# Kernel tuning notes

Hardware: AMD Instinct MI355X
Metric: run time of the kernel (lower is better)

The kernel has to match this reference:

```python
import jax, jax.numpy as jnp
import numpy as np

N = 50000
E = 800000
IN = 256
OUT = 32
H1 = 8
NEG_SLOPE = 0.2


def setup_inputs() -> dict:
    key = jax.random.key(0)
    ks = jax.random.split(key, 12)
    x = jax.random.normal(ks[0], (N, IN), dtype=jnp.float32)
    src = jax.random.randint(ks[1], (E,), 0, N, dtype=jnp.int32)
    dst = jax.random.randint(ks[2], (E,), 0, N, dtype=jnp.int32)
    s1 = 1.0 / np.sqrt(IN)
    s2 = 1.0 / np.sqrt(H1 * OUT)
    # layer 1 (8 heads, residual = Identity since IN == H1*OUT)
    W1 = jax.random.normal(ks[3], (IN, H1 * OUT), dtype=jnp.float32) * s1
    al1 = jax.random.normal(ks[4], (H1, OUT), dtype=jnp.float32) * s1
    ar1 = jax.random.normal(ks[5], (H1, OUT), dtype=jnp.float32) * s1
    b1 = jnp.zeros((H1 * OUT,), dtype=jnp.float32)
    # layer 2 (1 head, residual = Linear since H1*OUT != OUT)
    W2 = jax.random.normal(ks[6], (H1 * OUT, OUT), dtype=jnp.float32) * s2
    al2 = jax.random.normal(ks[7], (1, OUT), dtype=jnp.float32) * s2
    ar2 = jax.random.normal(ks[8], (1, OUT), dtype=jnp.float32) * s2
    resW2 = jax.random.normal(ks[9], (H1 * OUT, OUT), dtype=jnp.float32) * s2
    b2 = jnp.zeros((OUT,), dtype=jnp.float32)
    return {"x": x, "src": src, "dst": dst, "W1": W1, "al1": al1, "ar1": ar1,
            "b1": b1, "W2": W2, "al2": al2, "ar2": ar2, "resW2": resW2, "b2": b2}


def gat_layer(x, src, dst, W, al, ar, bias, heads, out_feats, res_fn):
    # x: (N, in). feat: (N, H, D)
    feat = (x @ W).reshape(N, heads, out_feats)
    el = jnp.sum(feat * al[None], axis=-1)  # (N, H)
    er = jnp.sum(feat * ar[None], axis=-1)  # (N, H)
    e = jax.nn.leaky_relu(el[src] + er[dst], NEG_SLOPE)  # (E, H)
    # edge softmax over incoming edges of each destination node
    emax = jax.ops.segment_max(e, dst, num_segments=N)  # (N, H)
    ee = jnp.exp(e - emax[dst])
    esum = jax.ops.segment_sum(ee, dst, num_segments=N)  # (N, H)
    a = ee / esum[dst]  # (E, H)
    # gather-multiply-scatter-add aggregation
    msg = feat[src] * a[..., None]  # (E, H, D)
    rst = jax.ops.segment_sum(msg, dst, num_segments=N)  # (N, H, D)
    rst = rst + res_fn(x)
    rst = rst + bias.reshape(1, heads, out_feats)
    return rst


def reference(x, src, dst, W1, al1, ar1, b1, W2, al2, ar2, resW2, b2):
    # layer 1: 8 heads, residual Identity (IN == H1*OUT)
    y = gat_layer(x, src, dst, W1, al1, ar1, b1, H1, OUT,
                  lambda h: h.reshape(N, H1, OUT))
    y = jax.nn.relu(y).reshape(N, H1 * OUT)
    # layer 2: 1 head, residual Linear projection
    y = gat_layer(y, src, dst, W2, al2, ar2, b2, 1, OUT,
                  lambda h: (h @ resW2).reshape(N, 1, OUT))
    return y
```

## Files before the change

### kernel.cpp

```cpp
#include <hip/hip_runtime.h>
#include <hip/hip_bf16.h>
#include <hip/hip_fp8.h>

#define N_NODES 50000
#define M_PAD   50048
#define N_EDGES 800000
#define NEG_SLOPE 0.2f

#define EPT 8
#define BKA 391
#define NBUCK 256
#define NPB 196
#define SEGCAP 40
#define GBLK 782

typedef __attribute__((ext_vector_type(8))) short bf16x8;
typedef __attribute__((ext_vector_type(4))) float f32x4;
typedef __attribute__((ext_vector_type(2))) float f32x2;

__device__ __forceinline__ unsigned short f2bf(float f) {
    unsigned u = __float_as_uint(f);
    u += 0x7FFFu + ((u >> 16) & 1u);
    return (unsigned short)(u >> 16);
}
__device__ __forceinline__ float bf2f(unsigned short h) {
    return __uint_as_float(((unsigned)h) << 16);
}

#if __has_builtin(__builtin_amdgcn_cvt_pk_f32_fp8)
__device__ __forceinline__ f32x2 fp8pk_lo(unsigned int p) { return __builtin_amdgcn_cvt_pk_f32_fp8(p, false); }
__device__ __forceinline__ f32x2 fp8pk_hi(unsigned int p) { return __builtin_amdgcn_cvt_pk_f32_fp8(p, true); }
#else
__device__ __forceinline__ float fp82f_s(unsigned char b) {
    __hip_fp8_e4m3 t; t.__x = (__hip_fp8_storage_t)b; return (float)t;
}
__device__ __forceinline__ f32x2 fp8pk_lo(unsigned int p) {
    f32x2 r; r.x = fp82f_s(p & 0xff); r.y = fp82f_s((p >> 8) & 0xff); return r;
}
__device__ __forceinline__ f32x2 fp8pk_hi(unsigned int p) {
    f32x2 r; r.x = fp82f_s((p >> 16) & 0xff); r.y = fp82f_s(p >> 24); return r;
}
#endif

#if __has_builtin(__builtin_amdgcn_cvt_pk_fp8_f32)
__device__ __forceinline__ unsigned int fp8enc2(float a, float b) {
    return (unsigned int)__builtin_amdgcn_cvt_pk_fp8_f32(a, b, 0, false);
}
#else
__device__ __forceinline__ unsigned int fp8enc2(float a, float b) {
    __hip_fp8_e4m3 ta(a), tb(b);
    return (unsigned int)ta.__x | ((unsigned int)tb.__x << 8);
}
#endif


__global__ __launch_bounds__(256) void k_trans(const float* __restrict__ W1, const float* __restrict__ W2,
                                               const float* __restrict__ resW2, const float* __restrict__ x,
                                               unsigned short* __restrict__ W1T, unsigned short* __restrict__ W2T,
                                               unsigned short* __restrict__ xb, unsigned int* __restrict__ btot) {
    int flat = blockIdx.y * 10 + blockIdx.x;
    if (flat == 0) btot[threadIdx.x] = 0;

    if (blockIdx.y < 8) {
        __shared__ unsigned short tile[32][33];
        int bx = blockIdx.x;
        const float* in;
        unsigned short* out;
        int Nn, n0;
        if (bx < 8)      { in = W1;    out = W1T;            Nn = 256; n0 = bx * 32; }
        else if (bx == 8){ in = W2;    out = W2T;            Nn = 32;  n0 = 0; }
        else             { in = resW2; out = W2T + 32 * 256; Nn = 32;  n0 = 0; }
        int k0 = blockIdx.y * 32;
        int tx = threadIdx.x & 31, ty = threadIdx.x >> 5;
        #pragma unroll
        for (int r = 0; r < 4; ++r) {
            int k = k0 + ty + r * 8;
            tile[ty + r * 8][tx] = f2bf(in[(size_t)k * Nn + n0 + tx]);
        }
        __syncthreads();
        #pragma unroll
        for (int r = 0; r < 4; ++r) {
            int n = ty + r * 8;
            out[(size_t)(n0 + n) * 256 + k0 + tx] = tile[tx][n];
        }
    } else {
        int xid = flat - 80;
        const size_t NCHUNK = (size_t)M_PAD * 256 / 8;
        for (size_t c = (size_t)xid * 256 + threadIdx.x; c < NCHUNK; c += (size_t)720 * 256) {
            size_t base = c * 8;
            float4 a = make_float4(0.f, 0.f, 0.f, 0.f), b = a;
            if (base < (size_t)N_NODES * 256) {
                a = *(const float4*)(x + base);
                b = *(const float4*)(x + base + 4);
            }
            ushort4 h0, h1;
            h0.x = f2bf(a.x); h0.y = f2bf(a.y); h0.z = f2bf(a.z); h0.w = f2bf(a.w);
            h1.x = f2bf(b.x); h1.y = f2bf(b.y); h1.z = f2bf(b.z); h1.w = f2bf(b.w);
            *(ushort4*)(xb + base) = h0;
            *(ushort4*)(xb + base + 4) = h1;
        }
    }
}


__device__ __forceinline__ void gemm1_half(int g, int bn0,
                                           const unsigned short* __restrict__ xb,
                                           const unsigned short* __restrict__ BT,
                                           const float* __restrict__ al1, const float* __restrict__ ar1,
                                           unsigned char* __restrict__ Cb8,
                                           float* __restrict__ el1, float* __restrict__ er1) {
    const int t = threadIdx.x;
    const int bm0 = g * 64;
    const int wave = t >> 6, lane = t & 63;
    const int wm = (wave & 1) * 32, wn = (wave >> 1) * 64;
    const int lm = lane & 15, quad = lane >> 4;

    f32x4 acc[2][4];
    #pragma unroll
    for (int i = 0; i < 2; ++i)
        #pragma unroll
        for (int j = 0; j < 4; ++j)
            #pragma unroll
            for (int r = 0; r < 4; ++r) acc[i][j][r] = 0.f;

    const unsigned short* bp[4];
    const unsigned short* ap[2];
    #pragma unroll
    for (int i = 0; i < 4; ++i)
        bp[i] = BT + (size_t)(bn0 + wn + i * 16 + lm) * 256 + quad * 8;
    #pragma unroll
    for (int i = 0; i < 2; ++i)
        ap[i] = xb + (size_t)(bm0 + wm + i * 16 + lm) * 256 + quad * 8;

    bf16x8 nb[4], na[2];
    #pragma unroll
    for (int i = 0; i < 4; ++i) nb[i] = *(const bf16x8*)(bp[i]);
    #pragma unroll
    for (int i = 0; i < 2; ++i) na[i] = *(const bf16x8*)(ap[i]);

    #pragma unroll
    for (int k0 = 0; k0 < 256; k0 += 32) {
        bf16x8 cb[4], ca[2];
        #pragma unroll
        for (int i = 0; i < 4; ++i) cb[i] = nb[i];
        #pragma unroll
        for (int i = 0; i < 2; ++i) ca[i] = na[i];
        if (k0 + 32 < 256) {
            #pragma unroll
            for (int i = 0; i < 4; ++i) nb[i] = *(const bf16x8*)(bp[i] + k0 + 32);
            #pragma unroll
            for (int i = 0; i < 2; ++i) na[i] = *(const bf16x8*)(ap[i] + k0 + 32);
        }
        #pragma unroll
        for (int mi = 0; mi < 2; ++mi)
            #pragma unroll
            for (int ni = 0; ni < 4; ++ni)
                acc[mi][ni] = __builtin_amdgcn_mfma_f32_16x16x32_bf16(ca[mi], cb[ni], acc[mi][ni], 0, 0, 0);
    }

    #pragma unroll
    for (int mi = 0; mi < 2; ++mi) {
        #pragma unroll
        for (int ni = 0; ni < 4; ++ni) {
            int col = bn0 + wn + ni * 16 + lm;
            int row0 = bm0 + wm + mi * 16 + quad * 4;
            unsigned int p01 = fp8enc2(acc[mi][ni][0], acc[mi][ni][1]);
            unsigned int p23 = fp8enc2(acc[mi][ni][2], acc[mi][ni][3]);
            Cb8[(size_t)(row0 + 0) * 256 + col] = (unsigned char)(p01 & 0xff);
            Cb8[(size_t)(row0 + 1) * 256 + col] = (unsigned char)((p01 >> 8) & 0xff);
            Cb8[(size_t)(row0 + 2) * 256 + col] = (unsigned char)(p23 & 0xff);
            Cb8[(size_t)(row0 + 3) * 256 + col] = (unsigned char)((p23 >> 8) & 0xff);
        }
    }
    float alv[4], arv[4];
    #pragma unroll
    for (int ni = 0; ni < 4; ++ni) {
        int colg = bn0 + wn + ni * 16 + lm;
        alv[ni] = al1[colg];
        arv[ni] = ar1[colg];
    }
    int head0 = (bn0 + wn) >> 5;
    #pragma unroll
    for (int gg = 0; gg < 2; ++gg) {
        #pragma unroll
        for (int mi = 0; mi < 2; ++mi) {
            #pragma unroll
            for (int r = 0; r < 4; ++r) {
                float pel = acc[mi][2 * gg][r] * alv[2 * gg] + acc[mi][2 * gg + 1][r] * alv[2 * gg + 1];
                float per = acc[mi][2 * gg][r] * arv[2 * gg] + acc[mi][2 * gg + 1][r] * arv[2 * gg + 1];
                #pragma unroll
                for (int m = 1; m <= 8; m <<= 1) {
                    pel += __shfl_xor(pel, m, 64);
                    per += __shfl_xor(per, m, 64);
                }
                if (lm == 0) {
                    int row = bm0 + wm + mi * 16 + quad * 4 + r;
                    el1[row * 8 + head0 + gg] = pel;
                    er1[row * 8 + head0 + gg] = per;
                }
            }
        }
    }
}


__global__ __launch_bounds__(512) void k_gemm1(const unsigned short* __restrict__ xb,
                                               const unsigned short* __restrict__ BT,
                                               const float* __restrict__ al1, const float* __restrict__ ar1,
                                               unsigned char* __restrict__ Cb8,
                                               float* __restrict__ el1, float* __restrict__ er1) {
    gemm1_half(blockIdx.x, 0, xb, BT, al1, ar1, Cb8, el1, er1);
}


__global__ __launch_bounds__(256) void k_bucketA(const int* __restrict__ src, const int* __restrict__ dst,
                                                 uint2* __restrict__ seg, unsigned int* __restrict__ cnt,
                                                 unsigned int* __restrict__ btot) {
    __shared__ unsigned int lcnt[NBUCK];
    int vb = blockIdx.x;
    lcnt[threadIdx.x] = 0;
    __syncthreads();
    int base = vb * (256 * EPT) + threadIdx.x;
    int sv[EPT], dv[EPT], bk[EPT], lr[EPT];
    #pragma unroll
    for (int q = 0; q < EPT; ++q) {
        int i = base + q * 256;
        if (i < N_EDGES) { sv[q] = src[i]; dv[q] = dst[i]; }
        else dv[q] = -1;
    }
    #pragma unroll
    for (int q = 0; q < EPT; ++q) {
        if (dv[q] >= 0) {
            bk[q] = (int)((unsigned)dv[q] / NPB);
            lr[q] = atomicAdd(&lcnt[bk[q]], 1u);
        }
    }
    __syncthreads();
    cnt[vb * NBUCK + threadIdx.x] = lcnt[threadIdx.x];
    if (lcnt[threadIdx.x] > 0) atomicAdd(&btot[threadIdx.x], lcnt[threadIdx.x]);
    #pragma unroll
    for (int q = 0; q < EPT; ++q) {
        if (dv[q] >= 0 && lr[q] < SEGCAP) {
            size_t slot = ((size_t)bk[q] * BKA + vb) * SEGCAP + lr[q];
            seg[slot] = make_uint2((unsigned)sv[q], (unsigned)dv[q] - (unsigned)bk[q] * NPB);
        }
    }
}


__global__ __launch_bounds__(256) void k_bucketB(const uint2* __restrict__ seg, const unsigned int* __restrict__ cnt,
                                                 const unsigned int* __restrict__ btot,
                                                 int* __restrict__ rowoff, int* __restrict__ csr_src) {
    __shared__ unsigned int hist[NPB];
    __shared__ unsigned int cursor[NPB];
    __shared__ unsigned int red[256];
    int b = blockIdx.x;
    int t = threadIdx.x;
    if (t < NPB) hist[t] = 0;
    red[t] = (t < b) ? btot[t] : 0;
    __syncthreads();
    #pragma unroll
    for (int off = 128; off > 0; off >>= 1) {
        if (t < off) red[t] += red[t + off];
        __syncthreads();
    }
    unsigned int base = red[0];
    __syncthreads();
    for (int s = t; s < BKA; s += 256) {
        unsigned int c = cnt[s * NBUCK + b];
        const uint2* sp = seg + ((size_t)b * BKA + s) * SEGCAP;
        for (unsigned int j = 0; j < c; ++j) {
            atomicAdd(&hist[sp[j].y], 1u);
        }
    }
    __syncthreads();
    red[t] = (t < NPB) ? hist[t] : 0;
    __syncthreads();
    for (int off = 1; off < 256; off <<= 1) {
        unsigned int val = (t >= off) ? red[t - off] : 0;
        __syncthreads();
        red[t] += val;
        __syncthreads();
    }
    if (t < NPB) {
        unsigned int excl = red[t] - hist[t];
        cursor[t] = excl;
        int v = b * NPB + t;
        if (v < N_NODES) rowoff[v] = (int)(base + excl);
    }
    if (b == NBUCK - 1 && t == 0) rowoff[N_NODES] = N_EDGES;
    __syncthreads();
    for (int s = t; s < BKA; s += 256) {
        unsigned int c = cnt[s * NBUCK + b];
        const uint2* sp = seg + ((size_t)b * BKA + s) * SEGCAP;
        for (unsigned int j = 0; j < c; ++j) {
            uint2 eg = sp[j];
            unsigned int r = atomicAdd(&cursor[eg.y], 1u);
            csr_src[base + r] = (int)eg.x;
        }
    }
}


__global__ __launch_bounds__(256) void k_agg1(const unsigned char* __restrict__ feat8,
                                              const float* __restrict__ el1, const float* __restrict__ er1,
                                              const unsigned short* __restrict__ xb, const float* __restrict__ b1,
                                              const int* __restrict__ rowoff, const int* __restrict__ csr_src,
                                              unsigned short* __restrict__ y_b) {
    int v = (blockIdx.x * 256 + threadIdx.x) >> 6;
    int lane = threadIdx.x & 63;
    if (v >= M_PAD) return;
    int c0 = lane * 4;
    if (v >= N_NODES) {
        ushort4 z = {0, 0, 0, 0};
        *(ushort4*)(y_b + (size_t)v * 256 + c0) = z;
        return;
    }
    int h = lane >> 3;
    float er  = er1[v * 8 + h];
    float erc = er1[v * 8 + (lane & 7)];
    float ax = 0.f, ay = 0.f, az = 0.f, aw = 0.f, wsum = 0.f;
    int s = rowoff[v], e = rowoff[v + 1];
    int j = s;
    for (; j + 7 < e; j += 8) {
        int um = csr_src[j + (lane >> 3)];
        float elv = el1[um * 8 + (lane & 7)];
        int u[8];
        #pragma unroll
        for (int q = 0; q < 8; ++q) u[q] = __shfl(um, q * 8);
        unsigned int hv[8];
        #pragma unroll
        for (int q = 0; q < 8; ++q) hv[q] = *(const unsigned int*)(feat8 + (size_t)u[q] * 256 + c0);
        float tq = elv + erc;
        tq = fmaxf(tq, NEG_SLOPE * tq);
        float wv = __expf(tq);
        #pragma unroll
        for (int q = 0; q < 8; ++q) {
            float w = __shfl(wv, q * 8 + h);
            wsum += w;
            f32x2 lo = fp8pk_lo(hv[q]);
            f32x2 hi = fp8pk_hi(hv[q]);
            ax += w * lo.x; ay += w * lo.y; az += w * hi.x; aw += w * hi.y;
        }
    }
    for (; j + 3 < e; j += 4) {
        int u[4];
        #pragma unroll
        for (int q = 0; q < 4; ++q) u[q] = csr_src[j + q];
        float tt[4];
        #pragma unroll
        for (int q = 0; q < 4; ++q) tt[q] = el1[u[q] * 8 + h] + er;
        unsigned int hv[4];
        #pragma unroll
        for (int q = 0; q < 4; ++q) hv[q] = *(const unsigned int*)(feat8 + (size_t)u[q] * 256 + c0);
        #pragma unroll
        for (int q = 0; q < 4; ++q) {
            float tq = fmaxf(tt[q], NEG_SLOPE * tt[q]);
            float w = __expf(tq);
            wsum += w;
            f32x2 lo = fp8pk_lo(hv[q]);
            f32x2 hi = fp8pk_hi(hv[q]);
            ax += w * lo.x; ay += w * lo.y; az += w * hi.x; aw += w * hi.y;
        }
    }
    for (; j < e; ++j) {
        int u = csr_src[j];
        float tt = el1[u * 8 + h] + er;
        unsigned int hh = *(const unsigned int*)(feat8 + (size_t)u * 256 + c0);
        tt = fmaxf(tt, NEG_SLOPE * tt);
        float w = __expf(tt);
        wsum += w;
        f32x2 lo = fp8pk_lo(hh);
        f32x2 hi = fp8pk_hi(hh);
        ax += w * lo.x; ay += w * lo.y; az += w * hi.x; aw += w * hi.y;
    }
    float inv = (e > s) ? 1.f / wsum : 0.f;
    ushort4 rh = *(const ushort4*)(xb + (size_t)v * 256 + c0);
    float4 bb = *(const float4*)(b1 + c0);
    ushort4 o;
    o.x = f2bf(fmaxf(ax * inv + bf2f(rh.x) + bb.x, 0.f));
    o.y = f2bf(fmaxf(ay * inv + bf2f(rh.y) + bb.y, 0.f));
    o.z = f2bf(fmaxf(az * inv + bf2f(rh.z) + bb.z, 0.f));
    o.w = f2bf(fmaxf(aw * inv + bf2f(rh.w) + bb.w, 0.f));
    *(ushort4*)(y_b + (size_t)v * 256 + c0) = o;
}


__global__ __launch_bounds__(256) void k_gemm2f(const unsigned short* __restrict__ Ab,
                                                const unsigned short* __restrict__ BT,
                                                const float* __restrict__ al2, const float* __restrict__ ar2,
                                                unsigned short* __restrict__ feat2b, float* __restrict__ res2,
                                                float* __restrict__ el2, float* __restrict__ er2) {
    const int t = threadIdx.x;
    const int bm0 = blockIdx.x * 64;
    const int wave = t >> 6, lane = t & 63;
    const int wm = (wave & 1) * 32, wn = (wave >> 1) * 32;
    const int lm = lane & 15, quad = lane >> 4;

    f32x4 acc[2][2];
    #pragma unroll
    for (int i = 0; i < 2; ++i)
        #pragma unroll
        for (int j = 0; j < 2; ++j)
            #pragma unroll
            for (int r = 0; r < 4; ++r) acc[i][j][r] = 0.f;

    const unsigned short* bp[2];
    const unsigned short* ap[2];
    #pragma unroll
    for (int i = 0; i < 2; ++i) {
        bp[i] = BT + (size_t)(wn + i * 16 + lm) * 256 + quad * 8;
        ap[i] = Ab + (size_t)(bm0 + wm + i * 16 + lm) * 256 + quad * 8;
    }

    bf16x8 nb[2], na[2];
    #pragma unroll
    for (int i = 0; i < 2; ++i) { nb[i] = *(const bf16x8*)(bp[i]); na[i] = *(const bf16x8*)(ap[i]); }

    #pragma unroll
    for (int k0 = 0; k0 < 256; k0 += 32) {
        bf16x8 cb[2], ca[2];
        #pragma unroll
        for (int i = 0; i < 2; ++i) { cb[i] = nb[i]; ca[i] = na[i]; }
        if (k0 + 32 < 256) {
            #pragma unroll
            for (int i = 0; i < 2; ++i) {
                nb[i] = *(const bf16x8*)(bp[i] + k0 + 32);
                na[i] = *(const bf16x8*)(ap[i] + k0 + 32);
            }
        }
        #pragma unroll
        for (int mi = 0; mi < 2; ++mi)
            #pragma unroll
            for (int ni = 0; ni < 2; ++ni)
                acc[mi][ni] = __builtin_amdgcn_mfma_f32_16x16x32_bf16(ca[mi], cb[ni], acc[mi][ni], 0, 0, 0);
    }

    #pragma unroll
    for (int mi = 0; mi < 2; ++mi) {
        #pragma unroll
        for (int ni = 0; ni < 2; ++ni) {
            int col = wn + ni * 16 + lm;
            #pragma unroll
            for (int r = 0; r < 4; ++r) {
                int row = bm0 + wm + mi * 16 + quad * 4 + r;
                float val = acc[mi][ni][r];
                if (col < 32) feat2b[(size_t)row * 32 + col] = f2bf(val);
                else          res2[(size_t)row * 32 + col - 32] = val;
            }
        }
    }
    if (wn == 0) {
        float alv[2], arv[2];
        #pragma unroll
        for (int ni = 0; ni < 2; ++ni) {
            alv[ni] = al2[ni * 16 + lm];
            arv[ni] = ar2[ni * 16 + lm];
        }
        #pragma unroll
        for (int mi = 0; mi < 2; ++mi) {
            #pragma unroll
            for (int r = 0; r < 4; ++r) {
                float pel = acc[mi][0][r] * alv[0] + acc[mi][1][r] * alv[1];
                float per = acc[mi][0][r] * arv[0] + acc[mi][1][r] * arv[1];
                #pragma unroll
                for (int m = 1; m <= 8; m <<= 1) {
                    pel += __shfl_xor(pel, m, 64);
                    per += __shfl_xor(per, m, 64);
                }
                if (lm == 0) {
                    int row = bm0 + wm + mi * 16 + quad * 4 + r;
                    el2[row] = pel;
                    er2[row] = per;
                }
            }
        }
    }
}


__global__ __launch_bounds__(256) void k_agg2(const unsigned short* __restrict__ feat2b,
                                              const float* __restrict__ el2, const float* __restrict__ er2,
                                              const float* __restrict__ res2, const float* __restrict__ b2,
                                              const int* __restrict__ rowoff, const int* __restrict__ csr_src,
                                              float* __restrict__ out) {
    int g = blockIdx.x * 256 + threadIdx.x;
    int v = g >> 5;
    int c = g & 31;
    if (v >= N_NODES) return;
    float er = er2[v];
    float acc = 0.f, wsum = 0.f;
    int s = rowoff[v], e = rowoff[v + 1];
    int j = s;
    for (; j + 3 < e; j += 4) {
        int u[4];
        #pragma unroll
        for (int q = 0; q < 4; ++q) u[q] = csr_src[j + q];
        float tt[4];
        #pragma unroll
        for (int q = 0; q < 4; ++q) tt[q] = el2[u[q]] + er;
        unsigned short fv[4];
        #pragma unroll
        for (int q = 0; q < 4; ++q) fv[q] = feat2b[(size_t)u[q] * 32 + c];
        #pragma unroll
        for (int q = 0; q < 4; ++q) {
            float tq = fmaxf(tt[q], NEG_SLOPE * tt[q]);
            float w = __expf(tq);
            wsum += w;
            acc += w * bf2f(fv[q]);
        }
    }
    for (; j < e; ++j) {
        int u = csr_src[j];
        float t = el2[u] + er;
        t = fmaxf(t, NEG_SLOPE * t);
        float w = __expf(t);
        wsum += w;
        acc += w * bf2f(feat2b[(size_t)u * 32 + c]);
    }
    float inv = (e > s) ? 1.f / wsum : 0.f;
    out[(size_t)v * 32 + c] = acc * inv + res2[(size_t)v * 32 + c] + b2[c];
}


extern "C" void kernel_launch(void* const* d_in, const int* in_sizes, int n_in,
                              void* d_out, int out_size, void* d_ws, size_t ws_size,
                              hipStream_t stream) {
    const float* x     = (const float*)d_in[0];
    const int*   src   = (const int*)d_in[1];
    const int*   dst   = (const int*)d_in[2];
    const float* W1    = (const float*)d_in[3];
    const float* al1   = (const float*)d_in[4];
    const float* ar1   = (const float*)d_in[5];
    const float* b1    = (const float*)d_in[6];
    const float* W2    = (const float*)d_in[7];
    const float* al2   = (const float*)d_in[8];
    const float* ar2   = (const float*)d_in[9];
    const float* resW2 = (const float*)d_in[10];
    const float* b2    = (const float*)d_in[11];
    float* out = (float*)d_out;

    char* ws = (char*)d_ws;
    size_t off = 0;
    auto alloc = [&](size_t bytes) {
        void* p = ws + off;
        off += (bytes + 255) & ~(size_t)255;
        return p;
    };
    unsigned short* xb     = (unsigned short*)alloc((size_t)M_PAD * 256 * 2);
    unsigned char*  feat8  = (unsigned char*)alloc((size_t)M_PAD * 256);
    unsigned short* y_b    = (unsigned short*)alloc((size_t)M_PAD * 256 * 2);
    unsigned short* W1T    = (unsigned short*)alloc((size_t)256 * 256 * 2);
    unsigned short* W2T    = (unsigned short*)alloc((size_t)64 * 256 * 2);
    unsigned short* feat2b = (unsigned short*)alloc((size_t)M_PAD * 32 * 2);
    float* res2   = (float*)alloc((size_t)M_PAD * 32 * 4);
    float* el1    = (float*)alloc((size_t)M_PAD * 8 * 4);
    float* er1    = (float*)alloc((size_t)M_PAD * 8 * 4);
    float* el2    = (float*)alloc((size_t)M_PAD * 4);
    float* er2    = (float*)alloc((size_t)M_PAD * 4);
    int*   rowoff = (int*)alloc((size_t)(N_NODES + 1) * 4);
    int*   csr    = (int*)alloc((size_t)N_EDGES * 4);
    uint2* seg    = (uint2*)alloc((size_t)NBUCK * BKA * SEGCAP * 8);
    unsigned int* cnt  = (unsigned int*)alloc((size_t)BKA * NBUCK * 4);
    unsigned int* btot = (unsigned int*)alloc((size_t)NBUCK * 4);
    (void)ws_size;

    k_trans<<<dim3(10, 80), 256, 0, stream>>>(W1, W2, resW2, x, W1T, W2T, xb, btot);

    k_bucketA<<<BKA, 256, 0, stream>>>(src, dst, seg, cnt, btot);

    k_gemm1<<<GBLK, 512, 0, stream>>>(xb, W1T, al1, ar1, feat8, el1, er1);

    k_bucketB<<<NBUCK, 256, 0, stream>>>(seg, cnt, btot, rowoff, csr);

    k_agg1<<<(M_PAD * 64) / 256, 256, 0, stream>>>(feat8, el1, er1, xb, b1, rowoff, csr, y_b);

    k_gemm2f<<<M_PAD / 64, 256, 0, stream>>>(y_b, W2T, al2, ar2, feat2b, res2, el2, er2);
    k_agg2<<<(N_NODES * 32) / 256, 256, 0, stream>>>(feat2b, el2, er2, res2, b2, rowoff, csr, out);
}
```

Baseline: 278.8 us.

## Stage A tile in LDS and pre-swizzle W1 into MFMA fragment order

W1 is now written by the transpose kernel in a fragment-ordered layout, so each lane's B operand for a k-step is one contiguous 16-byte load and a wave's loads are fully coalesced. The 64-row activation tile is loaded once into padded shared memory, and A fragments are read from LDS instead of strided global loads. The aim is to cut uncoalesced global traffic in the first-layer GEMM. In exchange it adds a block-wide sync and about 33KB of LDS per block, which may lower occupancy.

```diff
diff --git a/kernel.cpp b/kernel.cpp
--- a/kernel.cpp
+++ b/kernel.cpp
@@ -13,6 +13,7 @@
 #define NPB 196
 #define SEGCAP 40
 #define GBLK 782
+#define APAD 264
 
 typedef __attribute__((ext_vector_type(8))) short bf16x8;
 typedef __attribute__((ext_vector_type(4))) float f32x4;
@@ -56,7 +57,7 @@
 
 __global__ __launch_bounds__(256) void k_trans(const float* __restrict__ W1, const float* __restrict__ W2,
                                                const float* __restrict__ resW2, const float* __restrict__ x,
-                                               unsigned short* __restrict__ W1T, unsigned short* __restrict__ W2T,
+                                               unsigned short* __restrict__ W1F, unsigned short* __restrict__ W2T,
                                                unsigned short* __restrict__ xb, unsigned int* __restrict__ btot) {
     int flat = blockIdx.y * 10 + blockIdx.x;
     if (flat == 0) btot[threadIdx.x] = 0;
@@ -65,11 +66,10 @@
         __shared__ unsigned short tile[32][33];
         int bx = blockIdx.x;
         const float* in;
-        unsigned short* out;
         int Nn, n0;
-        if (bx < 8)      { in = W1;    out = W1T;            Nn = 256; n0 = bx * 32; }
-        else if (bx == 8){ in = W2;    out = W2T;            Nn = 32;  n0 = 0; }
-        else             { in = resW2; out = W2T + 32 * 256; Nn = 32;  n0 = 0; }
+        if (bx < 8)      { in = W1;    Nn = 256; n0 = bx * 32; }
+        else if (bx == 8){ in = W2;    Nn = 32;  n0 = 0; }
+        else             { in = resW2; Nn = 32;  n0 = 0; }
         int k0 = blockIdx.y * 32;
         int tx = threadIdx.x & 31, ty = threadIdx.x >> 5;
         #pragma unroll
@@ -81,7 +81,17 @@
         #pragma unroll
         for (int r = 0; r < 4; ++r) {
             int n = ty + r * 8;
-            out[(size_t)(n0 + n) * 256 + k0 + tx] = tile[tx][n];
+            unsigned short val = tile[tx][n];
+            int col = n0 + n;
+            int kk = k0 + tx;
+            if (bx < 8) {
+                size_t idx = (((size_t)(col >> 4) * 8 + (kk >> 5)) << 9)
+                           + ((((kk >> 3) & 3) * 16 + (col & 15)) << 3) + (kk & 7);
+                W1F[idx] = val;
+            } else {
+                unsigned short* out = (bx == 8) ? W2T : (W2T + 32 * 256);
+                out[(size_t)col * 256 + kk] = val;
+            }
         }
     } else {
         int xid = flat - 80;
@@ -103,18 +113,27 @@
 }
 
 
-__device__ __forceinline__ void gemm1_half(int g, int bn0,
-                                           const unsigned short* __restrict__ xb,
-                                           const unsigned short* __restrict__ BT,
-                                           const float* __restrict__ al1, const float* __restrict__ ar1,
-                                           unsigned char* __restrict__ Cb8,
-                                           float* __restrict__ el1, float* __restrict__ er1) {
+__global__ __launch_bounds__(512) void k_gemm1(const unsigned short* __restrict__ xb,
+                                               const unsigned short* __restrict__ W1F,
+                                               const float* __restrict__ al1, const float* __restrict__ ar1,
+                                               unsigned char* __restrict__ Cb8,
+                                               float* __restrict__ el1, float* __restrict__ er1) {
+    __shared__ unsigned short sA[64 * APAD];
     const int t = threadIdx.x;
-    const int bm0 = g * 64;
+    const int bm0 = blockIdx.x * 64;
     const int wave = t >> 6, lane = t & 63;
     const int wm = (wave & 1) * 32, wn = (wave >> 1) * 64;
     const int lm = lane & 15, quad = lane >> 4;
 
+    #pragma unroll
+    for (int rr = 0; rr < 4; ++rr) {
+        int ch = rr * 512 + t;
+        int row = ch >> 5, w = ch & 31;
+        bf16x8 vv = *(const bf16x8*)(xb + (size_t)(bm0 + row) * 256 + w * 8);
+        *(bf16x8*)(sA + row * APAD + w * 8) = vv;
+    }
+    __syncthreads();
+
     f32x4 acc[2][4];
     #pragma unroll
     for (int i = 0; i < 2; ++i)
@@ -124,33 +143,30 @@
             for (int r = 0; r < 4; ++r) acc[i][j][r] = 0.f;
 
     const unsigned short* bp[4];
+    #pragma unroll
+    for (int i = 0; i < 4; ++i)
+        bp[i] = W1F + ((size_t)((wave >> 1) * 4 + i)) * 4096 + lane * 8;
     const unsigned short* ap[2];
     #pragma unroll
-    for (int i = 0; i < 4; ++i)
-        bp[i] = BT + (size_t)(bn0 + wn + i * 16 + lm) * 256 + quad * 8;
-    #pragma unroll
     for (int i = 0; i < 2; ++i)
-        ap[i] = xb + (size_t)(bm0 + wm + i * 16 + lm) * 256 + quad * 8;
-
-    bf16x8 nb[4], na[2];
+        ap[i] = sA + (wm + i * 16 + lm) * APAD + quad * 8;
+
+    bf16x8 nb[4];
     #pragma unroll
     for (int i = 0; i < 4; ++i) nb[i] = *(const bf16x8*)(bp[i]);
-    #pragma unroll
-    for (int i = 0; i < 2; ++i) na[i] = *(const bf16x8*)(ap[i]);
-
-    #pragma unroll
-    for (int k0 = 0; k0 < 256; k0 += 32) {
-        bf16x8 cb[4], ca[2];
+
+    #pragma unroll
+    for (int q = 0; q < 8; ++q) {
+        bf16x8 cb[4];
         #pragma unroll
         for (int i = 0; i < 4; ++i) cb[i] = nb[i];
-        #pragma unroll
-        for (int i = 0; i < 2; ++i) ca[i] = na[i];
-        if (k0 + 32 < 256) {
-            #pragma unroll
-            for (int i = 0; i < 4; ++i) nb[i] = *(const bf16x8*)(bp[i] + k0 + 32);
-            #pragma unroll
-            for (int i = 0; i < 2; ++i) na[i] = *(const bf16x8*)(ap[i] + k0 + 32);
-        }
+        if (q < 7) {
+            #pragma unroll
+            for (int i = 0; i < 4; ++i) nb[i] = *(const bf16x8*)(bp[i] + (q + 1) * 512);
+        }
+        bf16x8 ca[2];
+        #pragma unroll
+        for (int i = 0; i < 2; ++i) ca[i] = *(const bf16x8*)(ap[i] + q * 32);
         #pragma unroll
         for (int mi = 0; mi < 2; ++mi)
             #pragma unroll
@@ -162,7 +178,7 @@
     for (int mi = 0; mi < 2; ++mi) {
         #pragma unroll
         for (int ni = 0; ni < 4; ++ni) {
-            int col = bn0 + wn + ni * 16 + lm;
+            int col = wn + ni * 16 + lm;
             int row0 = bm0 + wm + mi * 16 + quad * 4;
             unsigned int p01 = fp8enc2(acc[mi][ni][0], acc[mi][ni][1]);
             unsigned int p23 = fp8enc2(acc[mi][ni][2], acc[mi][ni][3]);
@@ -175,11 +191,11 @@
     float alv[4], arv[4];
     #pragma unroll
     for (int ni = 0; ni < 4; ++ni) {
-        int colg = bn0 + wn + ni * 16 + lm;
+        int colg = wn + ni * 16 + lm;
         alv[ni] = al1[colg];
         arv[ni] = ar1[colg];
     }
-    int head0 = (bn0 + wn) >> 5;
+    int head0 = wn >> 5;
     #pragma unroll
     for (int gg = 0; gg < 2; ++gg) {
         #pragma unroll
@@ -201,15 +217,6 @@
             }
         }
     }
-}
-
-
-__global__ __launch_bounds__(512) void k_gemm1(const unsigned short* __restrict__ xb,
-                                               const unsigned short* __restrict__ BT,
-                                               const float* __restrict__ al1, const float* __restrict__ ar1,
-                                               unsigned char* __restrict__ Cb8,
-                                               float* __restrict__ el1, float* __restrict__ er1) {
-    gemm1_half(blockIdx.x, 0, xb, BT, al1, ar1, Cb8, el1, er1);
 }
 
 
@@ -550,7 +557,7 @@
     unsigned short* xb     = (unsigned short*)alloc((size_t)M_PAD * 256 * 2);
     unsigned char*  feat8  = (unsigned char*)alloc((size_t)M_PAD * 256);
     unsigned short* y_b    = (unsigned short*)alloc((size_t)M_PAD * 256 * 2);
-    unsigned short* W1T    = (unsigned short*)alloc((size_t)256 * 256 * 2);
+    unsigned short* W1F    = (unsigned short*)alloc((size_t)256 * 256 * 2);
     unsigned short* W2T    = (unsigned short*)alloc((size_t)64 * 256 * 2);
     unsigned short* feat2b = (unsigned short*)alloc((size_t)M_PAD * 32 * 2);
     float* res2   = (float*)alloc((size_t)M_PAD * 32 * 4);
@@ -565,11 +572,11 @@
     unsigned int* btot = (unsigned int*)alloc((size_t)NBUCK * 4);
     (void)ws_size;
 
-    k_trans<<<dim3(10, 80), 256, 0, stream>>>(W1, W2, resW2, x, W1T, W2T, xb, btot);
+    k_trans<<<dim3(10, 80), 256, 0, stream>>>(W1, W2, resW2, x, W1F, W2T, xb, btot);
 
     k_bucketA<<<BKA, 256, 0, stream>>>(src, dst, seg, cnt, btot);
 
-    k_gemm1<<<GBLK, 512, 0, stream>>>(xb, W1T, al1, ar1, feat8, el1, er1);
+    k_gemm1<<<GBLK, 512, 0, stream>>>(xb, W1F, al1, ar1, feat8, el1, er1);
 
     k_bucketB<<<NBUCK, 256, 0, stream>>>(seg, cnt, btot, rowoff, csr);
 
```

Measured after the change: 251.0 us. 1.11x faster.
